# Kernel optimization log

Hardware: AMD Instinct MI355X
Metric: run time of the kernel (lower is better)

## Reference

```python
import jax, jax.numpy as jnp
import numpy as np

B = 256       # batch size
D = 128       # dim_s == dim_t == inputSize
OUT = 1000000 # outputSize (memory bank rows)
K = 511       # number of negatives (idx has K+1 columns)
MOM = 0.5     # momentum


def setup_inputs() -> dict:
    key = jax.random.key(0)
    ks = jax.random.split(key, 18)
    stdv = 1.0 / np.sqrt(D / 3.0)
    sc = 1.0 / np.sqrt(D)  # nn.Linear default init bound
    inp = {}
    inp["v1"] = jax.random.normal(ks[0], (B, D), jnp.float32)
    inp["v2"] = jax.random.normal(ks[1], (B, D), jnp.float32)
    y = jax.random.randint(ks[2], (B,), 0, OUT)
    inp["y"] = y
    idx = jax.random.randint(ks[3], (B, K + 1), 0, OUT)
    inp["idx"] = idx.at[:, 0].set(y)  # first column is the positive, as in torch
    inp["memory_v1"] = jax.random.uniform(ks[4], (OUT, D), jnp.float32, -stdv, stdv)
    inp["memory_v2"] = jax.random.uniform(ks[5], (OUT, D), jnp.float32, -stdv, stdv)
    names = ["Ws1", "bs1", "Ws2", "bs2", "Wsv", "bsv", "Wt1", "bt1", "Wt2", "bt2", "Wtv", "btv"]
    for i, n in enumerate(names):
        shape = (D, D) if n.startswith("W") else (D,)
        inp[n] = jax.random.uniform(ks[6 + i], shape, jnp.float32, -sc, sc)
    return inp


def _branch(v, w2, W1, b1, W2, b2, Wv, bv):
    # v: [B, D], w2: [K+1, B, D] (gathered memory rows, detached)
    a = v @ W1.T + b1                                 # [B, D]
    b_ = jnp.einsum('kbd,ed->kbe', w2, W2) + b2       # [K+1, B, D]
    h = jax.nn.relu(a[None, :, :] - b_)               # [K+1, B, D]
    return jnp.einsum('kbd,ed->kbe', h, Wv) + bv      # [K+1, B, D]


def reference(v1, v2, y, idx, memory_v1, memory_v2,
              Ws1, bs1, Ws2, bs2, Wsv, bsv, Wt1, bt1, Wt2, bt2, Wtv, btv):
    # gather K+1 memory rows per sample (detached in torch)
    w2 = jax.lax.stop_gradient(memory_v2[idx])        # [B, K+1, D]
    w2 = jnp.transpose(w2, (1, 0, 2))                 # [K+1, B, D]

    outs_s = _branch(v1, w2, Ws1, bs1, Ws2, bs2, Wsv, bsv)  # stacked outs_m_t_s
    outs_t = _branch(v2, w2, Wt1, bt1, Wt2, bt2, Wtv, btv)  # stacked outs_m_t

    # momentum normalize-and-scatter update (torch.no_grad block)
    def upd(mem, v):
        rows = mem[y] * MOM + v * (1.0 - MOM)                     # [B, D]
        rows = rows / jnp.sqrt(jnp.sum(rows * rows, axis=1, keepdims=True))
        return mem.at[y].set(rows)

    new_mem_v1 = jax.lax.stop_gradient(upd(memory_v1, v1))
    new_mem_v2 = jax.lax.stop_gradient(upd(memory_v2, v2))

    # torch returns (outs_m_t, outs_m_t_s) as lists; we stack them along K+1,
    # and additionally return the updated memory banks (the buffer side effect).
    return outs_t, outs_s, new_mem_v1, new_mem_v2
```

## Files before the change

### kernel.cpp

```cpp
#include <hip/hip_runtime.h>


typedef __attribute__((ext_vector_type(8))) short bf16x8;
typedef __attribute__((ext_vector_type(4))) float f32x4;
typedef __attribute__((ext_vector_type(4))) float fvec4;

__device__ __forceinline__ unsigned short f2bf(float f) {
    union { float ff; unsigned u; } v; v.ff = f;
    unsigned u = v.u;
    u += 0x7fffu + ((u >> 16) & 1u);
    return (unsigned short)(u >> 16);
}

__global__ void prep_weights(const float* __restrict__ Ws2,
                             const float* __restrict__ Wsv,
                             const float* __restrict__ Wt2,
                             const float* __restrict__ Wtv,
                             unsigned short* __restrict__ wb) {
    int i = blockIdx.x * 256 + threadIdx.x;
    if (i < 16384) {
        wb[i]         = f2bf(Ws2[i]);
        wb[16384 + i] = f2bf(Wsv[i]);
        wb[32768 + i] = f2bf(Wt2[i]);
        wb[49152 + i] = f2bf(Wtv[i]);
    }
}

__global__ void prep_a(const float* __restrict__ v1, const float* __restrict__ v2,
                       const float* __restrict__ Ws1, const float* __restrict__ bs1,
                       const float* __restrict__ bs2,
                       const float* __restrict__ Wt1, const float* __restrict__ bt1,
                       const float* __restrict__ bt2,
                       float* __restrict__ aS, float* __restrict__ aT) {
    __shared__ float vs1[128], vs2[128];
    const int b = blockIdx.x, e = threadIdx.x;
    vs1[e] = v1[b * 128 + e];
    vs2[e] = v2[b * 128 + e];
    __syncthreads();
    float s1 = 0.f, s2 = 0.f;
    const float4* w1 = (const float4*)(Ws1 + e * 128);
    const float4* w2 = (const float4*)(Wt1 + e * 128);
    #pragma unroll
    for (int d4 = 0; d4 < 32; ++d4) {
        float4 a = w1[d4], c = w2[d4];
        s1 += a.x * vs1[d4*4] + a.y * vs1[d4*4+1] + a.z * vs1[d4*4+2] + a.w * vs1[d4*4+3];
        s2 += c.x * vs2[d4*4] + c.y * vs2[d4*4+1] + c.z * vs2[d4*4+2] + c.w * vs2[d4*4+3];
    }
    aS[b * 128 + e] = s1 + bs1[e] - bs2[e];
    aT[b * 128 + e] = s2 + bt1[e] - bt2[e];
}

__device__ __forceinline__ void branch_body(
    int blk,
    const float* __restrict__ memv2, const int* __restrict__ idx,
    const float* __restrict__ aS, const float* __restrict__ aT,
    const unsigned short* __restrict__ wb,
    const float* __restrict__ bsv, const float* __restrict__ btv,
    float* __restrict__ outT, float* __restrict__ outS,
    unsigned short* Xs, unsigned short* Ht)
{
    const int tid  = threadIdx.x;
    const int wv   = tid >> 6, lane = tid & 63;
    const int m0   = blk * 128;
    const int b0   = m0 & 255;
    const int kq   = m0 >> 8;

    {
        const int sub = lane >> 5;
        const int c4  = (lane & 31) * 4;
        float4 xr[16];
        #pragma unroll
        for (int i = 0; i < 16; ++i) {
            const int r = wv * 32 + i * 2 + sub;
            const int grow = idx[(b0 + r) * 512 + kq];
            xr[i] = *(const float4*)(memv2 + (long)grow * 128 + c4);
        }
        #pragma unroll
        for (int i = 0; i < 16; ++i) {
            const int r = wv * 32 + i * 2 + sub;
            ushort4 u;
            u.x = f2bf(xr[i].x); u.y = f2bf(xr[i].y);
            u.z = f2bf(xr[i].z); u.w = f2bf(xr[i].w);
            *(ushort4*)&Xs[r * 128 + (c4 ^ ((r & 7) * 8))] = u;
        }
    }
    __syncthreads();

    const int r0   = wv * 32;
    const int lrow = lane & 15;
    const int kg   = lane >> 4;

    const unsigned short* Ws2b = wb;
    const unsigned short* Wsvb = wb + 16384;
    const unsigned short* Wt2b = wb + 32768;
    const unsigned short* Wtvb = wb + 49152;

    f32x4 accS[2][8], accT[2][8];
    #pragma unroll
    for (int mf = 0; mf < 2; ++mf)
        #pragma unroll
        for (int nf = 0; nf < 8; ++nf) {
            accS[mf][nf] = (f32x4){0.f, 0.f, 0.f, 0.f};
            accT[mf][nf] = (f32x4){0.f, 0.f, 0.f, 0.f};
        }

    #pragma unroll
    for (int kk = 0; kk < 4; ++kk) {
        const int kb = kk * 32 + kg * 8;
        const int ra = r0 + lrow, rb = r0 + 16 + lrow;
        bf16x8 A0 = *(const bf16x8*)&Xs[ra * 128 + (kb ^ ((ra & 7) * 8))];
        bf16x8 A1 = *(const bf16x8*)&Xs[rb * 128 + (kb ^ ((rb & 7) * 8))];
        #pragma unroll
        for (int nf = 0; nf < 8; ++nf) {
            const int e = nf * 16 + lrow;
            bf16x8 Bs = *(const bf16x8*)&Ws2b[e * 128 + kb];
            bf16x8 Bt = *(const bf16x8*)&Wt2b[e * 128 + kb];
            accS[0][nf] = __builtin_amdgcn_mfma_f32_16x16x32_bf16(A0, Bs, accS[0][nf], 0, 0, 0);
            accS[1][nf] = __builtin_amdgcn_mfma_f32_16x16x32_bf16(A1, Bs, accS[1][nf], 0, 0, 0);
            accT[0][nf] = __builtin_amdgcn_mfma_f32_16x16x32_bf16(A0, Bt, accT[0][nf], 0, 0, 0);
            accT[1][nf] = __builtin_amdgcn_mfma_f32_16x16x32_bf16(A1, Bt, accT[1][nf], 0, 0, 0);
        }
    }
    __syncthreads();

    #pragma unroll
    for (int mf = 0; mf < 2; ++mf) {
        #pragma unroll
        for (int nf = 0; nf < 8; ++nf) {
            const int e = nf * 16 + lrow;
            #pragma unroll
            for (int j = 0; j < 4; ++j) {
                const int rt = r0 + mf * 16 + kg * 4 + j;
                const int b  = b0 + rt;
                float hS = fmaxf(aS[b * 128 + e] - accS[mf][nf][j], 0.f);
                float hT = fmaxf(aT[b * 128 + e] - accT[mf][nf][j], 0.f);
                const int ei = e ^ ((rt & 7) * 8);
                Xs[rt * 128 + ei] = f2bf(hS);
                Ht[rt * 128 + ei] = f2bf(hT);
            }
        }
    }
    __syncthreads();

    f32x4 oS[2][8], oT[2][8];
    #pragma unroll
    for (int mf = 0; mf < 2; ++mf)
        #pragma unroll
        for (int nf = 0; nf < 8; ++nf) {
            oS[mf][nf] = (f32x4){0.f, 0.f, 0.f, 0.f};
            oT[mf][nf] = (f32x4){0.f, 0.f, 0.f, 0.f};
        }
    #pragma unroll
    for (int kk = 0; kk < 4; ++kk) {
        const int kb = kk * 32 + kg * 8;
        const int ra = r0 + lrow, rb = r0 + 16 + lrow;
        bf16x8 AS0 = *(const bf16x8*)&Xs[ra * 128 + (kb ^ ((ra & 7) * 8))];
        bf16x8 AS1 = *(const bf16x8*)&Xs[rb * 128 + (kb ^ ((rb & 7) * 8))];
        bf16x8 AT0 = *(const bf16x8*)&Ht[ra * 128 + (kb ^ ((ra & 7) * 8))];
        bf16x8 AT1 = *(const bf16x8*)&Ht[rb * 128 + (kb ^ ((rb & 7) * 8))];
        #pragma unroll
        for (int nf = 0; nf < 8; ++nf) {
            const int e = nf * 16 + lrow;
            bf16x8 Bs = *(const bf16x8*)&Wsvb[e * 128 + kb];
            bf16x8 Bt = *(const bf16x8*)&Wtvb[e * 128 + kb];
            oS[0][nf] = __builtin_amdgcn_mfma_f32_16x16x32_bf16(AS0, Bs, oS[0][nf], 0, 0, 0);
            oS[1][nf] = __builtin_amdgcn_mfma_f32_16x16x32_bf16(AS1, Bs, oS[1][nf], 0, 0, 0);
            oT[0][nf] = __builtin_amdgcn_mfma_f32_16x16x32_bf16(AT0, Bt, oT[0][nf], 0, 0, 0);
            oT[1][nf] = __builtin_amdgcn_mfma_f32_16x16x32_bf16(AT1, Bt, oT[1][nf], 0, 0, 0);
        }
    }

    float bvS[8], bvT[8];
    #pragma unroll
    for (int nf = 0; nf < 8; ++nf) {
        bvS[nf] = bsv[nf * 16 + lrow];
        bvT[nf] = btv[nf * 16 + lrow];
    }
    #pragma unroll
    for (int mf = 0; mf < 2; ++mf) {
        #pragma unroll
        for (int nf = 0; nf < 8; ++nf) {
            const int e = nf * 16 + lrow;
            #pragma unroll
            for (int j = 0; j < 4; ++j) {
                const int rt = r0 + mf * 16 + kg * 4 + j;
                const long off = (long)(m0 + rt) * 128 + e;
                __builtin_nontemporal_store(oT[mf][nf][j] + bvT[nf], outT + off);
                __builtin_nontemporal_store(oS[mf][nf][j] + bvS[nf], outS + off);
            }
        }
    }
}

__device__ __forceinline__ void copy_body(
    int cid, const float* __restrict__ mv1, const float* __restrict__ mv2,
    float* __restrict__ oM1, float* __restrict__ oM2)
{
    const bool bank2 = (cid >= 1000);
    const long base = (long)(bank2 ? cid - 1000 : cid) * 32000;
    const fvec4* src = (bank2 ? (const fvec4*)mv2 : (const fvec4*)mv1) + base;
    fvec4* dst = (bank2 ? (fvec4*)oM2 : (fvec4*)oM1) + base;
    const int t = threadIdx.x;
    #pragma unroll 1
    for (int i = 0; i < 125; i += 25) {
        fvec4 v[25];
        #pragma unroll
        for (int u = 0; u < 25; ++u) {
            const fvec4* p = src + (long)(i + u) * 256 + t;
            v[u] = bank2 ? *p : __builtin_nontemporal_load(p);
        }
        #pragma unroll
        for (int u = 0; u < 25; ++u)
            __builtin_nontemporal_store(v[u], dst + (long)(i + u) * 256 + t);
    }
}

__global__ __launch_bounds__(256) void mega(
    const float* __restrict__ memv2, const int* __restrict__ idx,
    const float* __restrict__ aS, const float* __restrict__ aT,
    const unsigned short* __restrict__ wb,
    const float* __restrict__ bsv, const float* __restrict__ btv,
    float* __restrict__ outT, float* __restrict__ outS,
    const float* __restrict__ mv1,
    float* __restrict__ oM1, float* __restrict__ oM2)
{
    __shared__ unsigned short Xs[128 * 128];
    __shared__ unsigned short Ht[128 * 128];
    const int bid = blockIdx.x;
    const int r3 = bid % 3;
    if (r3 == 0) {
        branch_body(bid / 3, memv2, idx, aS, aT, wb, bsv, btv, outT, outS, Xs, Ht);
    } else {
        const int cid = (bid / 3) * 2 + (r3 - 1);
        if (cid < 2000)
            copy_body(cid, mv1, memv2, oM1, oM2);
    }
}

__global__ void update_mem(const float* __restrict__ v1, const float* __restrict__ v2,
                           const int* __restrict__ y,
                           const float* __restrict__ m1, const float* __restrict__ m2,
                           float* __restrict__ o1, float* __restrict__ o2) {
    __shared__ int s_skip;
    __shared__ float part1[2], part2[2];
    const int b = blockIdx.x, t = threadIdx.x;
    const int yb = y[b];
    if (t == 0) {
        int sk = 0;
        for (int b2 = b + 1; b2 < 256; ++b2) sk |= (y[b2] == yb);
        s_skip = sk;
    }
    __syncthreads();
    if (s_skip) return;
    float x1 = m1[(long)yb * 128 + t] * 0.5f + v1[b * 128 + t] * 0.5f;
    float x2 = m2[(long)yb * 128 + t] * 0.5f + v2[b * 128 + t] * 0.5f;
    float s1 = x1 * x1, s2 = x2 * x2;
    #pragma unroll
    for (int o = 32; o > 0; o >>= 1) {
        s1 += __shfl_down(s1, o);
        s2 += __shfl_down(s2, o);
    }
    if ((t & 63) == 0) { part1[t >> 6] = s1; part2[t >> 6] = s2; }
    __syncthreads();
    const float n1 = part1[0] + part1[1];
    const float n2 = part2[0] + part2[1];
    o1[(long)yb * 128 + t] = x1 / sqrtf(n1);
    o2[(long)yb * 128 + t] = x2 / sqrtf(n2);
}

extern "C" void kernel_launch(void* const* d_in, const int* in_sizes, int n_in,
                              void* d_out, int out_size, void* d_ws, size_t ws_size,
                              hipStream_t stream) {
    (void)in_sizes; (void)n_in; (void)out_size; (void)ws_size;
    const float* v1  = (const float*)d_in[0];
    const float* v2  = (const float*)d_in[1];
    const int*   y   = (const int*)d_in[2];
    const int*   idx = (const int*)d_in[3];
    const float* mv1 = (const float*)d_in[4];
    const float* mv2 = (const float*)d_in[5];
    const float* Ws1 = (const float*)d_in[6];
    const float* bs1 = (const float*)d_in[7];
    const float* Ws2 = (const float*)d_in[8];
    const float* bs2 = (const float*)d_in[9];
    const float* Wsv = (const float*)d_in[10];
    const float* bsv = (const float*)d_in[11];
    const float* Wt1 = (const float*)d_in[12];
    const float* bt1 = (const float*)d_in[13];
    const float* Wt2 = (const float*)d_in[14];
    const float* bt2 = (const float*)d_in[15];
    const float* Wtv = (const float*)d_in[16];
    const float* btv = (const float*)d_in[17];

    float* outT = (float*)d_out;
    float* outS = outT + 16777216;
    float* oM1  = outT + 33554432;
    float* oM2  = oM1 + 128000000;

    float* aS = (float*)d_ws;
    float* aT = aS + 32768;
    unsigned short* wb = (unsigned short*)(aT + 32768);

    prep_weights<<<64, 256, 0, stream>>>(Ws2, Wsv, Wt2, Wtv, wb);
    prep_a<<<256, 128, 0, stream>>>(v1, v2, Ws1, bs1, bs2, Wt1, bt1, bt2, aS, aT);
    mega<<<3072, 256, 0, stream>>>(mv2, idx, aS, aT, wb, bsv, btv, outT, outS,
                                   mv1, oM1, oM2);
    update_mem<<<256, 128, 0, stream>>>(v1, v2, y, mv1, mv2, oM1, oM2);
}
```

Measured before the change: 461.7 us.

## Split mega kernel into per-wave roles mixing branch GEMM and bank copy

Each block now runs one wave computing a 32-row branch tile and three waves copying memory-bank slices. Previously, whole blocks did either GEMM or copy. This shrinks shared memory per block, removes block-level barriers, and interleaves compute and streaming copy within each CU. In exchange, each weight tile is reloaded four times as often and per-wave copy chunks carry bounds checks.

```diff
diff --git a/kernel.cpp b/kernel.cpp
--- a/kernel.cpp
+++ b/kernel.cpp
@@ -50,8 +50,8 @@
     aT[b * 128 + e] = s2 + bt1[e] - bt2[e];
 }
 
-__device__ __forceinline__ void branch_body(
-    int blk,
+__device__ __forceinline__ void branch_wave(
+    int bid, int lane,
     const float* __restrict__ memv2, const int* __restrict__ idx,
     const float* __restrict__ aS, const float* __restrict__ aT,
     const unsigned short* __restrict__ wb,
@@ -59,34 +59,30 @@
     float* __restrict__ outT, float* __restrict__ outS,
     unsigned short* Xs, unsigned short* Ht)
 {
-    const int tid  = threadIdx.x;
-    const int wv   = tid >> 6, lane = tid & 63;
-    const int m0   = blk * 128;
-    const int b0   = m0 & 255;
-    const int kq   = m0 >> 8;
-
+    const int m0 = bid * 32;
+    const int b0 = m0 & 255;
+    const int kq = m0 >> 8;
+
+    const int sub = lane >> 5;
+    const int c4  = (lane & 31) * 4;
     {
-        const int sub = lane >> 5;
-        const int c4  = (lane & 31) * 4;
         float4 xr[16];
         #pragma unroll
         for (int i = 0; i < 16; ++i) {
-            const int r = wv * 32 + i * 2 + sub;
+            const int r = i * 2 + sub;
             const int grow = idx[(b0 + r) * 512 + kq];
             xr[i] = *(const float4*)(memv2 + (long)grow * 128 + c4);
         }
         #pragma unroll
         for (int i = 0; i < 16; ++i) {
-            const int r = wv * 32 + i * 2 + sub;
+            const int r = i * 2 + sub;
             ushort4 u;
             u.x = f2bf(xr[i].x); u.y = f2bf(xr[i].y);
             u.z = f2bf(xr[i].z); u.w = f2bf(xr[i].w);
             *(ushort4*)&Xs[r * 128 + (c4 ^ ((r & 7) * 8))] = u;
         }
     }
-    __syncthreads();
-
-    const int r0   = wv * 32;
+
     const int lrow = lane & 15;
     const int kg   = lane >> 4;
 
@@ -107,7 +103,7 @@
     #pragma unroll
     for (int kk = 0; kk < 4; ++kk) {
         const int kb = kk * 32 + kg * 8;
-        const int ra = r0 + lrow, rb = r0 + 16 + lrow;
+        const int ra = lrow, rb = 16 + lrow;
         bf16x8 A0 = *(const bf16x8*)&Xs[ra * 128 + (kb ^ ((ra & 7) * 8))];
         bf16x8 A1 = *(const bf16x8*)&Xs[rb * 128 + (kb ^ ((rb & 7) * 8))];
         #pragma unroll
@@ -121,7 +117,6 @@
             accT[1][nf] = __builtin_amdgcn_mfma_f32_16x16x32_bf16(A1, Bt, accT[1][nf], 0, 0, 0);
         }
     }
-    __syncthreads();
 
     #pragma unroll
     for (int mf = 0; mf < 2; ++mf) {
@@ -130,7 +125,7 @@
             const int e = nf * 16 + lrow;
             #pragma unroll
             for (int j = 0; j < 4; ++j) {
-                const int rt = r0 + mf * 16 + kg * 4 + j;
+                const int rt = mf * 16 + kg * 4 + j;
                 const int b  = b0 + rt;
                 float hS = fmaxf(aS[b * 128 + e] - accS[mf][nf][j], 0.f);
                 float hT = fmaxf(aT[b * 128 + e] - accT[mf][nf][j], 0.f);
@@ -140,7 +135,6 @@
             }
         }
     }
-    __syncthreads();
 
     f32x4 oS[2][8], oT[2][8];
     #pragma unroll
@@ -153,7 +147,7 @@
     #pragma unroll
     for (int kk = 0; kk < 4; ++kk) {
         const int kb = kk * 32 + kg * 8;
-        const int ra = r0 + lrow, rb = r0 + 16 + lrow;
+        const int ra = lrow, rb = 16 + lrow;
         bf16x8 AS0 = *(const bf16x8*)&Xs[ra * 128 + (kb ^ ((ra & 7) * 8))];
         bf16x8 AS1 = *(const bf16x8*)&Xs[rb * 128 + (kb ^ ((rb & 7) * 8))];
         bf16x8 AT0 = *(const bf16x8*)&Ht[ra * 128 + (kb ^ ((ra & 7) * 8))];
@@ -170,48 +164,51 @@
         }
     }
 
-    float bvS[8], bvT[8];
-    #pragma unroll
-    for (int nf = 0; nf < 8; ++nf) {
-        bvS[nf] = bsv[nf * 16 + lrow];
-        bvT[nf] = btv[nf * 16 + lrow];
-    }
     #pragma unroll
     for (int mf = 0; mf < 2; ++mf) {
         #pragma unroll
         for (int nf = 0; nf < 8; ++nf) {
             const int e = nf * 16 + lrow;
+            const float bS = bsv[e], bT = btv[e];
             #pragma unroll
             for (int j = 0; j < 4; ++j) {
-                const int rt = r0 + mf * 16 + kg * 4 + j;
+                const int rt = mf * 16 + kg * 4 + j;
                 const long off = (long)(m0 + rt) * 128 + e;
-                __builtin_nontemporal_store(oT[mf][nf][j] + bvT[nf], outT + off);
-                __builtin_nontemporal_store(oS[mf][nf][j] + bvS[nf], outS + off);
+                __builtin_nontemporal_store(oT[mf][nf][j] + bT, outT + off);
+                __builtin_nontemporal_store(oS[mf][nf][j] + bS, outS + off);
             }
         }
     }
 }
 
-__device__ __forceinline__ void copy_body(
-    int cid, const float* __restrict__ mv1, const float* __restrict__ mv2,
-    float* __restrict__ oM1, float* __restrict__ oM2)
+template <bool CACHED>
+__device__ __forceinline__ void copy_wave_impl(
+    long w, int lane, const fvec4* __restrict__ src, fvec4* __restrict__ dst)
 {
-    const bool bank2 = (cid >= 1000);
-    const long base = (long)(bank2 ? cid - 1000 : cid) * 32000;
-    const fvec4* src = (bank2 ? (const fvec4*)mv2 : (const fvec4*)mv1) + base;
-    fvec4* dst = (bank2 ? (fvec4*)oM2 : (fvec4*)oM1) + base;
-    const int t = threadIdx.x;
+    const long f0 = w * 5248 + lane;
     #pragma unroll 1
-    for (int i = 0; i < 125; i += 25) {
-        fvec4 v[25];
-        #pragma unroll
-        for (int u = 0; u < 25; ++u) {
-            const fvec4* p = src + (long)(i + u) * 256 + t;
-            v[u] = bank2 ? *p : __builtin_nontemporal_load(p);
-        }
-        #pragma unroll
-        for (int u = 0; u < 25; ++u)
-            __builtin_nontemporal_store(v[u], dst + (long)(i + u) * 256 + t);
+    for (int kb = 0; kb < 80; kb += 8) {
+        fvec4 v[8];
+        long ff[8];
+        #pragma unroll
+        for (int u = 0; u < 8; ++u) {
+            const long f = f0 + (long)(kb + u) * 64;
+            ff[u] = f;
+            if (f < 32000000)
+                v[u] = CACHED ? src[f] : __builtin_nontemporal_load(src + f);
+        }
+        #pragma unroll
+        for (int u = 0; u < 8; ++u)
+            if (ff[u] < 32000000)
+                __builtin_nontemporal_store(v[u], dst + ff[u]);
+    }
+    #pragma unroll
+    for (int k = 80; k < 82; ++k) {
+        const long f = f0 + (long)k * 64;
+        if (f < 32000000) {
+            fvec4 v = CACHED ? src[f] : __builtin_nontemporal_load(src + f);
+            __builtin_nontemporal_store(v, dst + f);
+        }
     }
 }
 
@@ -224,16 +221,19 @@
     const float* __restrict__ mv1,
     float* __restrict__ oM1, float* __restrict__ oM2)
 {
-    __shared__ unsigned short Xs[128 * 128];
-    __shared__ unsigned short Ht[128 * 128];
-    const int bid = blockIdx.x;
-    const int r3 = bid % 3;
-    if (r3 == 0) {
-        branch_body(bid / 3, memv2, idx, aS, aT, wb, bsv, btv, outT, outS, Xs, Ht);
+    __shared__ unsigned short Xs[32 * 128];
+    __shared__ unsigned short Ht[32 * 128];
+    const int bid  = blockIdx.x;
+    const int wv   = threadIdx.x >> 6;
+    const int lane = threadIdx.x & 63;
+    if (wv == 0) {
+        branch_wave(bid, lane, memv2, idx, aS, aT, wb, bsv, btv, outT, outS, Xs, Ht);
     } else {
-        const int cid = (bid / 3) * 2 + (r3 - 1);
-        if (cid < 2000)
-            copy_body(cid, mv1, memv2, oM1, oM2);
+        const long cw = (long)bid * 3 + (wv - 1);
+        if (cw < 6144)
+            copy_wave_impl<false>(cw, lane, (const fvec4*)mv1, (fvec4*)oM1);
+        else
+            copy_wave_impl<true>(cw - 6144, lane, (const fvec4*)memv2, (fvec4*)oM2);
     }
 }
 
@@ -302,7 +302,7 @@
 
     prep_weights<<<64, 256, 0, stream>>>(Ws2, Wsv, Wt2, Wtv, wb);
     prep_a<<<256, 128, 0, stream>>>(v1, v2, Ws1, bs1, bs2, Wt1, bt1, bt2, aS, aT);
-    mega<<<3072, 256, 0, stream>>>(mv2, idx, aS, aT, wb, bsv, btv, outT, outS,
+    mega<<<4096, 256, 0, stream>>>(mv2, idx, aS, aT, wb, bsv, btv, outT, outS,
                                    mv1, oM1, oM2);
     update_mem<<<256, 128, 0, stream>>>(v1, v2, y, mv1, mv2, oM1, oM2);
 }
```

Measured after the change: 931.0 us. 2.02x slower.
